# Optimization experiments

Measured on AMD Instinct MI355X. Metric: run time of the kernel, lower is better.

Reference implementation:

```python
import jax, jax.numpy as jnp
import numpy as np

# Static config matching init_kwargs
COUT, CIN, K = 64, 64, 3
PAD = K // 2  # padding=1


def setup_inputs() -> dict:
    key = jax.random.key(0)
    k1, k2, k3 = jax.random.split(key, 3)
    B, H, W, FH, FW, SC = 2, 256, 256, 16, 16, 128
    hyper_params = COUT * CIN * K * K  # 36864
    x = jax.random.normal(k1, (B, CIN, H, W), jnp.float32)
    s = jax.random.normal(k2, (B, SC, FH, FW), jnp.float32)
    s2w = jax.random.normal(k3, (hyper_params, SC), jnp.float32) * 0.02
    return {"x": x, "s": s, "s2w": s2w}


def reference(x, s, s2w):
    """HyperPatchConv2d forward: per-patch dynamically generated 3x3 conv.

    x:   [b, c, h, w]   input feature map
    s:   [b, sc, fh, fw] hypernetwork signal (one vector per patch)
    s2w: [P, sc]         signal2weights 1x1 conv (P = out*cin*k*k)
    """
    b, c, h, w = x.shape
    fh, fw = s.shape[-2:]
    ph, pw = h // fh, w // fw          # patch size
    kh, kw = ph + 2 * PAD, pw + 2 * PAD  # unfold window (patch + halo)

    # signal2weights: 1x1 conv -> per-patch flattened conv weight
    wflat = jnp.einsum('pc,bcfg->bfgp', s2w, s)            # [b,fh,fw,P]
    Wdyn = wflat.reshape(b, fh, fw, COUT, CIN, K, K)        # per-patch conv kernels

    # reflect-pad then unfold into overlapping (kh,kw) patches, stride (ph,pw)
    xp = jnp.pad(x, ((0, 0), (0, 0), (PAD, PAD), (PAD, PAD)), mode='reflect')
    idx_h = (jnp.arange(fh) * ph)[:, None] + jnp.arange(kh)[None, :]  # [fh,kh]
    idx_w = (jnp.arange(fw) * pw)[:, None] + jnp.arange(kw)[None, :]  # [fw,kw]
    patches = xp[:, :, idx_h][:, :, :, :, idx_w]            # [b,c,fh,kh,fw,kw]

    # extract KxK sliding windows inside each patch (valid conv, stride 1)
    wi = jnp.arange(ph)[:, None] + jnp.arange(K)[None, :]   # [ph,K]
    wj = jnp.arange(pw)[:, None] + jnp.arange(K)[None, :]   # [pw,K]
    win = patches[:, :, :, wi]                              # [b,c,fh,ph,K,fw,kw]
    win = win[:, :, :, :, :, :, wj]                         # [b,c,fh,ph,K,fw,pw,K]
    win = win.transpose(0, 2, 5, 1, 3, 4, 6, 7)             # [b,fh,fw,c,ph,K,pw,K]

    # per-patch dynamic conv
    out = jnp.einsum('bfgocij,bfgcpiqj->bfgopq', Wdyn, win)  # [b,fh,fw,o,ph,pw]

    # fold: non-overlapping reassembly (stride == patch size)
    return out.transpose(0, 3, 1, 4, 2, 5).reshape(b, COUT, h, w)
```

## Files before the change

### kernel.cpp

```cpp
#include <hip/hip_runtime.h>
#include <hip/hip_bf16.h>


#define C_OUT 64
#define C_IN  64
#define P_TOTAL 36864
#define N_PATCH 512
#define WSTR 72
#define CSTR3 72

typedef __bf16 bf16x8 __attribute__((ext_vector_type(8)));
typedef float  f32x4  __attribute__((ext_vector_type(4)));

__device__ __forceinline__ unsigned short f2bf(float f) {
  unsigned int u = __float_as_uint(f);
  u += 0x7fffu + ((u >> 16) & 1u);
  return (unsigned short)(u >> 16);
}
__device__ __forceinline__ unsigned int pack2(float a, float b) {
  return (unsigned int)f2bf(a) | ((unsigned int)f2bf(b) << 16);
}
__device__ __forceinline__ void gll16(const void* g, void* l) {
  __builtin_amdgcn_global_load_lds(
      (const __attribute__((address_space(1))) void*)g,
      (__attribute__((address_space(3))) void*)l, 16, 0, 0);
}

__global__ __launch_bounds__(256) void prep_ws(
    const float* __restrict__ s, const float* __restrict__ s2w,
    unsigned short* __restrict__ sTg, unsigned short* __restrict__ s2wP) {
  const int bid = blockIdx.x;
  const int t = threadIdx.x;

  if (bid < 32) {
    const int sb = bid >> 4;
    const int g = bid & 15;
    float v[8];
    #pragma unroll
    for (int e = 0; e < 8; ++e)
      v[e] = s[((size_t)(sb * 128 + g * 8 + e)) * 256 + t];
    uint4 o;
    o.x = pack2(v[0], v[1]); o.y = pack2(v[2], v[3]);
    o.z = pack2(v[4], v[5]); o.w = pack2(v[6], v[7]);
    const int ntile = sb * 2 + (t >> 7);
    const int slot = (t & 127) ^ (g & 7);
    *(uint4*)(sTg + ((size_t)(ntile * 2048 + g * 128 + slot)) * 8) = o;
    return;
  }

  const int b3 = bid - 32;
  const int m = b3 * 64 + (t >> 2);
  const int q = t & 3;
  const int j = m & 7;
  const int lane6 = (m >> 3) & 63;
  const int fragidx = m >> 9;
  const int tap = fragidx >> 3;
  const int ksH = (fragidx >> 2) & 1;
  const int mtH = fragidx & 3;
  const int co = mtH * 16 + (lane6 & 15);
  const int ci = ksH * 32 + (lane6 >> 4) * 8 + j;
  const int p = co * 576 + ci * 9 + tap;
  const float* src = s2w + (size_t)p * 128 + q * 32;
  const int mtile = m >> 7;
  const int r128 = m & 127;
  #pragma unroll
  for (int gg = 0; gg < 4; ++gg) {
    const int g = q * 4 + gg;
    const float4 v0 = *(const float4*)(src + gg * 8);
    const float4 v1 = *(const float4*)(src + gg * 8 + 4);
    uint4 o;
    o.x = pack2(v0.x, v0.y); o.y = pack2(v0.z, v0.w);
    o.z = pack2(v1.x, v1.y); o.w = pack2(v1.z, v1.w);
    const int slot = r128 ^ (g & 7);
    *(uint4*)(s2wP + ((size_t)(mtile * 2048 + g * 128 + slot)) * 8) = o;
  }
}

__global__ __launch_bounds__(256) void wgen_plus(
    const float* __restrict__ x,
    const unsigned short* __restrict__ s2wP,
    const unsigned short* __restrict__ sTg,
    unsigned short* __restrict__ xT,
    unsigned short* __restrict__ wout)
{
  __shared__ unsigned short lds[16640];
  const int bid = blockIdx.x;
  const int tid = threadIdx.x;

  if (bid < 512) {
    const int bb = bid >> 8, row = bid & 255;
    unsigned short* xl = lds;
    #pragma unroll
    for (int it = 0; it < 16; ++it) {
      const int ci = it * 4 + (tid >> 6);
      const int px = (tid & 63) * 4;
      const float4 v = *(const float4*)(x + ((size_t)(bb * 64 + ci)) * 65536 + row * 256 + px);
      ushort4 o;
      o.x = f2bf(v.x); o.y = f2bf(v.y); o.z = f2bf(v.z); o.w = f2bf(v.w);
      *(ushort4*)&xl[ci * 260 + px] = o;
    }
    __syncthreads();
    unsigned short* dst = xT + ((size_t)((bb << 16) + (row << 8) + tid)) * 64;
    #pragma unroll
    for (int k8 = 0; k8 < 8; ++k8) {
      const unsigned int w0 = (unsigned int)xl[(k8 * 8 + 0) * 260 + tid] |
                              ((unsigned int)xl[(k8 * 8 + 1) * 260 + tid] << 16);
      const unsigned int w1 = (unsigned int)xl[(k8 * 8 + 2) * 260 + tid] |
                              ((unsigned int)xl[(k8 * 8 + 3) * 260 + tid] << 16);
      const unsigned int w2 = (unsigned int)xl[(k8 * 8 + 4) * 260 + tid] |
                              ((unsigned int)xl[(k8 * 8 + 5) * 260 + tid] << 16);
      const unsigned int w3 = (unsigned int)xl[(k8 * 8 + 6) * 260 + tid] |
                              ((unsigned int)xl[(k8 * 8 + 7) * 260 + tid] << 16);
      *(uint4*)(dst + k8 * 8) = make_uint4(w0, w1, w2, w3);
    }
    return;
  }

  const int bid2 = bid - 512;
  const int n = bid2 / 576;
  const int mt = bid2 - n * 576;
  const int m0 = mt * 64;
  const int n0 = n * 64;
  unsigned short* As = lds;
  unsigned short* Bs = lds + 8192;

  const unsigned short* srcA = s2wP + (size_t)(mt >> 1) * 16384 + (mt & 1) * 512;
  const unsigned short* srcB = sTg + (size_t)(n >> 1) * 16384 + (n & 1) * 512;
  #pragma unroll
  for (int i = 0; i < 4; ++i) {
    const int c = i * 256 + tid;
    const int g = c >> 6;
    gll16(srcA + (size_t)(g * 1024 + (c & 63) * 8), As + c * 8);
  }
  #pragma unroll
  for (int i = 0; i < 4; ++i) {
    const int c = i * 256 + tid;
    const int g = c >> 6;
    gll16(srcB + (size_t)(g * 1024 + (c & 63) * 8), Bs + c * 8);
  }
  __syncthreads();

  const int w = tid >> 6;
  const int lane = tid & 63;
  const int col = lane & 15;
  const int quad = lane >> 4;

  f32x4 acc[4] = {};
  #pragma unroll
  for (int ks = 0; ks < 4; ++ks) {
    const int g = ks * 4 + quad;
    const int gb = g * 512;
    const int gx = (g & 7) * 8;
    const bf16x8 afr = *(const bf16x8*)&As[gb + (((w * 16 + col) * 8) ^ gx)];
    bf16x8 bfr[4];
    #pragma unroll
    for (int nt = 0; nt < 4; ++nt)
      bfr[nt] = *(const bf16x8*)&Bs[gb + (((nt * 16 + col) * 8) ^ gx)];
    #pragma unroll
    for (int nt = 0; nt < 4; ++nt)
      acc[nt] = __builtin_amdgcn_mfma_f32_16x16x32_bf16(afr, bfr[nt], acc[nt], 0, 0, 0);
  }
  __syncthreads();

  unsigned short* Ct = lds;
  const int mloc = w * 16 + quad * 4;
  #pragma unroll
  for (int nt = 0; nt < 4; ++nt) {
    const int pl = nt * 16 + col;
    ushort4 o;
    o.x = f2bf(acc[nt][0]); o.y = f2bf(acc[nt][1]);
    o.z = f2bf(acc[nt][2]); o.w = f2bf(acc[nt][3]);
    *(ushort4*)&Ct[pl * CSTR3 + mloc] = o;
  }
  __syncthreads();
  #pragma unroll
  for (int i = 0; i < 2; ++i) {
    const int chunk = i * 256 + tid;
    const int pl = chunk >> 3;
    const int ii = chunk & 7;
    const uint4 v = *(const uint4*)&Ct[pl * CSTR3 + ii * 8];
    *(uint4*)(wout + (size_t)(n0 + pl) * P_TOTAL + m0 + ii * 8) = v;
  }
}

__global__ __launch_bounds__(512, 2) void conv_kernel(
    const unsigned short* __restrict__ xT,
    const unsigned short* __restrict__ wfrag,
    float* __restrict__ out)
{
  __shared__ unsigned short win[324 * WSTR];
  const int tid = threadIdx.x;
  const int patch = blockIdx.x;
  const int bb = patch >> 8;
  const int fg = patch & 255;
  const int f = fg >> 4, g = fg & 15;
  const int row0 = f * 16, col0 = g * 16;

  for (int chunk = tid; chunk < 2592; chunk += 512) {
    const int cell = chunk >> 3;
    const int j = chunk & 7;
    const int r = cell / 18;
    const int c = cell - r * 18;
    int rr = row0 + r - 1; rr = rr < 0 ? -rr : (rr > 255 ? 510 - rr : rr);
    int cc = col0 + c - 1; cc = cc < 0 ? -cc : (cc > 255 ? 510 - cc : cc);
    *(uint4*)&win[cell * WSTR + j * 8] =
        *(const uint4*)(xT + ((size_t)((bb << 16) + (rr << 8) + cc)) * 64 + j * 8);
  }
  __syncthreads();

  const int wave = tid >> 6;
  const int lane = tid & 63;
  const int t = lane & 15;
  const int quad = lane >> 4;
  const int mh = wave & 1;
  const int rq = wave >> 1;

  f32x4 acc[2][4] = {};
  const bf16x8* wb = (const bf16x8*)(wfrag + (size_t)patch * P_TOTAL);

  #pragma unroll
  for (int tap = 0; tap < 9; ++tap) {
    const int ti = tap / 3;
    const int tj = tap - ti * 3;
    bf16x8 afr[2][2];
    #pragma unroll
    for (int ks = 0; ks < 2; ++ks)
      #pragma unroll
      for (int ml = 0; ml < 2; ++ml)
        afr[ks][ml] = wb[((tap * 2 + ks) * 4 + mh * 2 + ml) * 64 + lane];

    #pragma unroll
    for (int nt = 0; nt < 4; ++nt) {
      const int r = rq * 4 + nt + ti;
      const int c = t + tj;
      const int base = (r * 18 + c) * WSTR + quad * 8;
      #pragma unroll
      for (int ks = 0; ks < 2; ++ks) {
        const bf16x8 bfr = *(const bf16x8*)&win[base + ks * 32];
        acc[0][nt] = __builtin_amdgcn_mfma_f32_16x16x32_bf16(afr[ks][0], bfr, acc[0][nt], 0, 0, 0);
        acc[1][nt] = __builtin_amdgcn_mfma_f32_16x16x32_bf16(afr[ks][1], bfr, acc[1][nt], 0, 0, 0);
      }
    }
  }

  #pragma unroll
  for (int ml = 0; ml < 2; ++ml) {
    #pragma unroll
    for (int nt = 0; nt < 4; ++nt) {
      const int p = row0 + rq * 4 + nt;
      #pragma unroll
      for (int reg = 0; reg < 4; ++reg) {
        const int co = (mh * 2 + ml) * 16 + quad * 4 + reg;
        out[(((size_t)bb * C_OUT + co) << 16) + ((size_t)p << 8) + col0 + t] = acc[ml][nt][reg];
      }
    }
  }
}

extern "C" void kernel_launch(void* const* d_in, const int* in_sizes, int n_in,
                              void* d_out, int out_size, void* d_ws, size_t ws_size,
                              hipStream_t stream) {
  const float* x   = (const float*)d_in[0];
  const float* s   = (const float*)d_in[1];
  const float* s2w = (const float*)d_in[2];
  float* out = (float*)d_out;

  char* ws = (char*)d_ws;
  unsigned short* wbuf = (unsigned short*)(ws);
  unsigned short* sTg  = (unsigned short*)(ws + 37748736);
  unsigned short* xT   = (unsigned short*)(ws + 37879808);
  unsigned short* s2wP = (unsigned short*)(ws + 54657024);

  prep_ws<<<608, 256, 0, stream>>>(s, s2w, sTg, s2wP);
  wgen_plus<<<5120, 256, 0, stream>>>(x, s2wP, sTg, xT, wbuf);
  conv_kernel<<<N_PATCH, 512, 0, stream>>>(xT, wbuf, out);
}
```

Baseline: 128.9 us.

## Stream per-patch weights through LDS double buffer and remap wave tiling

The conv kernel now prefetches each tap's weight fragments into a two-slot LDS ring with async global-to-LDS loads, overlapping the next tap's load with the current tap's MFMAs. Before, every wave read them straight from global memory into registers. Wave work is also remapped: each wave owns one 16-channel output tile across 8 pixel rows instead of two channel tiles across 4 rows. This cuts redundant weight fetches per wave but adds a block-wide barrier per tap and raises LDS use, which may limit occupancy. The synchronisation looks thin, since the first tap's ring slot may be read without an explicit wait on the async load.

```diff
diff --git a/kernel.cpp b/kernel.cpp
--- a/kernel.cpp
+++ b/kernel.cpp
@@ -188,13 +188,18 @@
     const unsigned short* __restrict__ wfrag,
     float* __restrict__ out)
 {
-  __shared__ unsigned short win[324 * WSTR];
+  __shared__ unsigned short lds[23328 + 8192];
+  unsigned short* win = lds;
+  unsigned short* ring = lds + 23328;
   const int tid = threadIdx.x;
   const int patch = blockIdx.x;
   const int bb = patch >> 8;
   const int fg = patch & 255;
   const int f = fg >> 4, g = fg & 15;
   const int row0 = f * 16, col0 = g * 16;
+  const unsigned short* wp = wfrag + (size_t)patch * P_TOTAL;
+
+  gll16(wp + tid * 8, ring + tid * 8);
 
   for (int chunk = tid; chunk < 2592; chunk += 512) {
     const int cell = chunk >> 3;
@@ -212,47 +217,41 @@
   const int lane = tid & 63;
   const int t = lane & 15;
   const int quad = lane >> 4;
-  const int mh = wave & 1;
-  const int rq = wave >> 1;
-
-  f32x4 acc[2][4] = {};
-  const bf16x8* wb = (const bf16x8*)(wfrag + (size_t)patch * P_TOTAL);
+  const int mt = wave & 3;
+  const int ph = wave >> 2;
+
+  f32x4 acc[8] = {};
 
   #pragma unroll
   for (int tap = 0; tap < 9; ++tap) {
+    if (tap < 8)
+      gll16(wp + (size_t)(tap + 1) * 4096 + tid * 8,
+            ring + ((tap + 1) & 1) * 4096 + tid * 8);
+    const int cur = (tap & 1) * 4096;
     const int ti = tap / 3;
     const int tj = tap - ti * 3;
-    bf16x8 afr[2][2];
-    #pragma unroll
-    for (int ks = 0; ks < 2; ++ks)
-      #pragma unroll
-      for (int ml = 0; ml < 2; ++ml)
-        afr[ks][ml] = wb[((tap * 2 + ks) * 4 + mh * 2 + ml) * 64 + lane];
-
-    #pragma unroll
-    for (int nt = 0; nt < 4; ++nt) {
-      const int r = rq * 4 + nt + ti;
+    const bf16x8 afr0 = *(const bf16x8*)&ring[cur + mt * 512 + lane * 8];
+    const bf16x8 afr1 = *(const bf16x8*)&ring[cur + (4 + mt) * 512 + lane * 8];
+    #pragma unroll
+    for (int nt = 0; nt < 8; ++nt) {
+      const int r = ph * 8 + nt + ti;
       const int c = t + tj;
       const int base = (r * 18 + c) * WSTR + quad * 8;
-      #pragma unroll
-      for (int ks = 0; ks < 2; ++ks) {
-        const bf16x8 bfr = *(const bf16x8*)&win[base + ks * 32];
-        acc[0][nt] = __builtin_amdgcn_mfma_f32_16x16x32_bf16(afr[ks][0], bfr, acc[0][nt], 0, 0, 0);
-        acc[1][nt] = __builtin_amdgcn_mfma_f32_16x16x32_bf16(afr[ks][1], bfr, acc[1][nt], 0, 0, 0);
-      }
-    }
-  }
-
-  #pragma unroll
-  for (int ml = 0; ml < 2; ++ml) {
-    #pragma unroll
-    for (int nt = 0; nt < 4; ++nt) {
-      const int p = row0 + rq * 4 + nt;
-      #pragma unroll
-      for (int reg = 0; reg < 4; ++reg) {
-        const int co = (mh * 2 + ml) * 16 + quad * 4 + reg;
-        out[(((size_t)bb * C_OUT + co) << 16) + ((size_t)p << 8) + col0 + t] = acc[ml][nt][reg];
-      }
+      const bf16x8 b0 = *(const bf16x8*)&win[base];
+      const bf16x8 b1 = *(const bf16x8*)&win[base + 32];
+      acc[nt] = __builtin_amdgcn_mfma_f32_16x16x32_bf16(afr0, b0, acc[nt], 0, 0, 0);
+      acc[nt] = __builtin_amdgcn_mfma_f32_16x16x32_bf16(afr1, b1, acc[nt], 0, 0, 0);
+    }
+    __syncthreads();
+  }
+
+  #pragma unroll
+  for (int nt = 0; nt < 8; ++nt) {
+    const int p = row0 + ph * 8 + nt;
+    #pragma unroll
+    for (int reg = 0; reg < 4; ++reg) {
+      const int co = mt * 16 + quad * 4 + reg;
+      out[(((size_t)bb * C_OUT + co) << 16) + ((size_t)p << 8) + col0 + t] = acc[nt][reg];
     }
   }
 }
```

New measurement: 127.5 us. No clear change (-1.1%).
